# Kernel optimization log

Measured on AMD Instinct MI355X. Metric: run time of the kernel, lower is better.

## Reference

```python
import jax, jax.numpy as jnp
import numpy as np

Q_LEN = 2048
K_LEN = 2048
BATCH = 2
EMBED = 1024
HEADS = 16
HEAD_DIM = EMBED // HEADS
PE_ROWS = 2 * K_LEN


def _shift(p):
    # Transformer-XL pad/flatten shift: p is [B, H, Q, S] with S = 2*K-1 -> [B, H, Q, K]
    B, H, Q, S = p.shape
    pp = jnp.pad(p, ((0, 0), (0, 0), (0, 1), (0, 1)))          # [B,H,Q+1,S+1]
    flat = pp.reshape(B, H, (Q + 1) * (S + 1))
    flat = jax.lax.slice_in_dim(flat, S // 2, S // 2 + Q * S, axis=-1)
    return flat.reshape(B, H, Q, S)[..., : (S + 1) // 2]


def setup_inputs() -> dict:
    key = jax.random.key(0)
    ks = jax.random.split(key, 11)
    ws = 0.02  # weight scale
    inp = {
        "query": jax.random.normal(ks[0], (Q_LEN, BATCH, EMBED), jnp.float32),
        "key": jax.random.normal(ks[1], (K_LEN, BATCH, EMBED), jnp.float32),
        "value": jax.random.normal(ks[2], (K_LEN, BATCH, EMBED), jnp.float32),
        "pe": jax.random.normal(ks[3], (PE_ROWS, EMBED), jnp.float32),
        "w_q": jax.random.normal(ks[4], (EMBED, EMBED), jnp.float32) * ws,
        "w_k": jax.random.normal(ks[5], (EMBED, EMBED), jnp.float32) * ws,
        "w_v": jax.random.normal(ks[6], (EMBED, EMBED), jnp.float32) * ws,
        "w_k_pos": jax.random.normal(ks[7], (EMBED, EMBED), jnp.float32) * ws,
        "out_proj": jax.random.normal(ks[8], (EMBED, EMBED), jnp.float32) * ws,
        "content_bias": jax.random.normal(ks[9], (HEADS, HEAD_DIM), jnp.float32) * ws,
        "pos_bias": jax.random.normal(ks[10], (HEADS, HEAD_DIM), jnp.float32) * ws,
        "attn_mask": jnp.triu(jnp.ones((Q_LEN, K_LEN), dtype=bool), k=1),  # causal
    }
    return inp


def reference(query, key, value, pe, w_q, w_k, w_v, w_k_pos, out_proj,
              content_bias, pos_bias, attn_mask):
    Qlen, B, E = query.shape
    Klen = key.shape[0]
    H, D = content_bias.shape
    scaling = D ** -0.5

    # projections (torch Linear: x @ W^T); layout -> [B, H, L, D]
    q = (query @ w_q.T).reshape(Qlen, B, H, D).transpose(1, 2, 0, 3)
    k = (key @ w_k.T).reshape(Klen, B, H, D).transpose(1, 2, 0, 3)
    v = (value @ w_v.T).reshape(Klen, B, H, D).transpose(1, 2, 0, 3)

    # relative position keys: pe slice of size 2K-1 starting at pe.size(0)//2 - K + 1
    lower = pe.shape[0] // 2 - Klen + 1
    pe_slice = jax.lax.dynamic_slice_in_dim(pe, lower, 2 * Klen - 1, axis=0)
    k_pos = (pe_slice @ w_k_pos.T).reshape(2 * Klen - 1, H, D).transpose(1, 0, 2)  # [H, 2K-1, D]

    content = jnp.einsum('bhqd,bhkd->bhqk', q + content_bias[None, :, None, :], k)
    pos = jnp.einsum('bhqd,hsd->bhqs', q + pos_bias[None, :, None, :], k_pos)
    pos = _shift(pos)  # [B, H, Q, K]

    attn = (content + pos) * scaling
    attn = jnp.where(attn_mask[None, None], -jnp.inf, attn)
    w = jax.nn.softmax(attn, axis=-1)

    out = jnp.einsum('bhqk,bhkd->bhqd', w, v)
    out = out.transpose(2, 0, 1, 3).reshape(Qlen, B, E)
    return out @ out_proj.T
```

## Files before the change

### kernel.cpp

```cpp
#include <hip/hip_runtime.h>
#include <hip/hip_bf16.h>

typedef __hip_bfloat16 bf16;
typedef __attribute__((ext_vector_type(8))) short short8;
typedef __attribute__((ext_vector_type(8))) unsigned short u16x8;
typedef __attribute__((ext_vector_type(4))) float f32x4;

#define QL   2048
#define KLEN 2048
#define BATCH 2
#define EMB  1024
#define NH   16
#define HD   64
#define SPE  4095

__device__ __forceinline__ int detect_f32_wave(const void* __restrict__ p) {
    const ushort4 v = ((const ushort4*)p)[threadIdx.x & 63];
    int c = 0;
    c += __popcll(__ballot(((v.x >> 7) & 0xFF) >= 0x8A));
    c += __popcll(__ballot(((v.y >> 7) & 0xFF) >= 0x8A));
    c += __popcll(__ballot(((v.z >> 7) & 0xFF) >= 0x8A));
    c += __popcll(__ballot(((v.w >> 7) & 0xFF) >= 0x8A));
    return c >= 8;
}

__device__ __forceinline__ ushort4 cvt4(const void* src, long u4i, int f32) {
    ushort4 o;
    if (f32) {
        float4 v = ((const float4*)src)[u4i];
        bf16 a = (bf16)v.x, b = (bf16)v.y, c = (bf16)v.z, e = (bf16)v.w;
        o.x = *(unsigned short*)&a; o.y = *(unsigned short*)&b;
        o.z = *(unsigned short*)&c; o.w = *(unsigned short*)&e;
    } else {
        o = ((const ushort4*)src)[u4i];
    }
    return o;
}

__global__ __launch_bounds__(256) void conv_w(
    const void* w0, const void* w1, const void* w2, const void* w3, const void* w4,
    const void* cb, const void* pb, bf16* __restrict__ wdst)
{
    const int t = threadIdx.x;
    const int bid = blockIdx.x;
    __shared__ int f32s;
    if (bid < 1280) {
        const int seg = bid >> 8, inner = bid & 255;
        const void* src = seg == 0 ? w0 : seg == 1 ? w1 : seg == 2 ? w2 : seg == 3 ? w3 : w4;
        bf16* d = wdst + (size_t)seg * 1048576;
        if (t < 64) { int r = detect_f32_wave(src); if (t == 0) f32s = r; }
        __syncthreads();
        const int f32 = f32s;
#pragma unroll
        for (int i = 0; i < 4; i++) {
            long u4i = (long)inner * 1024 + i * 256 + t;
            ((ushort4*)d)[u4i] = cvt4(src, u4i, f32);
        }
    } else {
        if (t < 64) { int r = detect_f32_wave(cb); if (t == 0) f32s = r; }
        __syncthreads();
        const int f32 = f32s;
        ((ushort4*)(wdst + 5242880))[t]        = cvt4(cb, t, f32);
        ((ushort4*)(wdst + 5242880 + 1024))[t] = cvt4(pb, t, f32);
    }
}

__device__ __forceinline__ void llds16(const bf16* g, bf16* l) {
    __builtin_amdgcn_global_load_lds(
        (const __attribute__((address_space(1))) void*)g,
        (__attribute__((address_space(3))) void*)l,
        16, 0, 0);
}

__device__ __forceinline__ short8 pack_f32x8(const float4& a, const float4& b) {
    short8 o; bf16 x;
    x = (bf16)a.x; o[0] = *(short*)&x;  x = (bf16)a.y; o[1] = *(short*)&x;
    x = (bf16)a.z; o[2] = *(short*)&x;  x = (bf16)a.w; o[3] = *(short*)&x;
    x = (bf16)b.x; o[4] = *(short*)&x;  x = (bf16)b.y; o[5] = *(short*)&x;
    x = (bf16)b.z; o[6] = *(short*)&x;  x = (bf16)b.w; o[7] = *(short*)&x;
    return o;
}

template<bool F32>
struct AStage {
    u16x8  u[2];
    float4 f[2][2];
    __device__ __forceinline__ void load(const void* Av, const int go[2], int k0) {
#pragma unroll
        for (int i = 0; i < 2; i++) {
            int e = go[i] + k0;
            if (F32) {
                const float4* F = (const float4*)Av;
                f[i][0] = F[e >> 2];
                f[i][1] = F[(e >> 2) + 1];
            } else {
                u[i] = ((const u16x8*)Av)[e >> 3];
            }
        }
    }
    __device__ __forceinline__ void write(bf16* dst, int t) {
#pragma unroll
        for (int i = 0; i < 2; i++) {
            int c = i * 256 + t;
            short8 v;
            if (F32) v = pack_f32x8(f[i][0], f[i][1]);
            else     v = *(short8*)&u[i];
            *(short8*)&dst[c * 8] = v;
        }
    }
};

__device__ __forceinline__ void gcompute(
    const bf16* As, const bf16* Ws, int wr, int wc, int lm, int quad,
    f32x4 acc[4][8])
{
    short8 af[4], wf[8];
#pragma unroll
    for (int x = 0; x < 4; x++) {
        int ra = wr + x * 16 + lm;
        af[x] = *(const short8*)&As[ra * 32 + ((quad ^ (ra & 3)) * 8)];
    }
#pragma unroll
    for (int y = 0; y < 8; y++) {
        int rb = wc + y * 16 + lm;
        wf[y] = *(const short8*)&Ws[rb * 32 + ((quad ^ (rb & 3)) * 8)];
    }
#pragma unroll
    for (int mt = 0; mt < 4; mt++)
#pragma unroll
        for (int nt = 0; nt < 8; nt++)
            acc[mt][nt] = __builtin_amdgcn_mfma_f32_16x16x32_bf16(
                af[mt], wf[nt], acc[mt][nt], 0, 0, 0);
}

#define GWB() do { asm volatile("s_waitcnt vmcnt(0) lgkmcnt(0)" ::: "memory"); \
    __builtin_amdgcn_s_barrier(); __builtin_amdgcn_sched_barrier(0); } while (0)
#define GLB() do { asm volatile("s_waitcnt lgkmcnt(0)" ::: "memory"); \
    __builtin_amdgcn_s_barrier(); __builtin_amdgcn_sched_barrier(0); } while (0)

template<bool F32>
__device__ void gloop(
    const void* Av, const bf16* W, int m0, int n0, int mode,
    bf16* Asd0, bf16* Asd1, bf16* Wsd0, bf16* Wsd1,
    int t, int wr, int wc, int lm, int quad, f32x4 acc[4][8])
{
    int go[2];
#pragma unroll
    for (int i = 0; i < 2; i++) {
        int c = i * 256 + t, r = c >> 2, gc = (c & 3) ^ (r & 3);
        int ar = m0 + r;
        if (mode == 3) { ar = ar + 1; if (ar > 4095) ar = 4095; }
        go[i] = ar * 1024 + gc * 8;
    }
    auto stageW = [&](bf16* dst, int k0) {
#pragma unroll
        for (int i = 0; i < 4; i++) {
            int c = i * 256 + t, r = c >> 2, gc = (c & 3) ^ (r & 3);
            llds16(W + (size_t)(n0 + r) * 1024 + k0 + gc * 8, dst + (c & ~63) * 8);
        }
    };

    AStage<F32> sa, sb;
    sa.load(Av, go, 0);
    stageW(Wsd0, 0);

#pragma unroll 1
    for (int tt = 0; tt < 32; tt += 2) {
        GWB();
        sa.write(Asd0, t);
        GLB();
        sb.load(Av, go, (tt + 1) * 32);
        stageW(Wsd1, (tt + 1) * 32);
        gcompute(Asd0, Wsd0, wr, wc, lm, quad, acc);

        GWB();
        sb.write(Asd1, t);
        GLB();
        if (tt + 2 < 32) {
            sa.load(Av, go, (tt + 2) * 32);
            stageW(Wsd0, (tt + 2) * 32);
        }
        gcompute(Asd1, Wsd1, wr, wc, lm, quad, acc);
    }
}

__global__ __launch_bounds__(256, 2) void gemm_big(
    const void* __restrict__ Aq, const void* __restrict__ Ak,
    const void* __restrict__ Avv, const void* __restrict__ Ape,
    const bf16* __restrict__ ao, const bf16* __restrict__ wslab,
    bf16* __restrict__ qc, bf16* __restrict__ qp,
    bf16* __restrict__ kw, bf16* __restrict__ vw,
    bf16* __restrict__ kpos, float* __restrict__ outf, int mode_base)
{
    const int o = blockIdx.x;
    const int mode = mode_base + (o >> 7);
    const int s = (o >> 3) & 15;
    const int bx = (o & 7) + 8 * (s & 3);
    const int by = s >> 2;

    const void* A = mode == 0 ? Aq : mode == 1 ? Ak : mode == 2 ? Avv :
                    mode == 3 ? Ape : (const void*)ao;
    const bf16* W = wslab + (size_t)mode * 1048576;

    __shared__ __align__(16) bf16 Asd[2][128 * 32];
    __shared__ __align__(16) bf16 Wsd[2][256 * 32];
    __shared__ int f32s;

    const int t = threadIdx.x;
    const int w = t >> 6, lane = t & 63, lm = lane & 15, quad = lane >> 4;
    const int m0 = bx * 128, n0 = by * 256;
    const int wr = (w >> 1) * 64, wc = (w & 1) * 128;

    if (t < 64) { int r = detect_f32_wave(A); if (t == 0) f32s = r; }
    __syncthreads();

    f32x4 acc[4][8] = {};

    if (f32s) gloop<true >(A, W, m0, n0, mode, Asd[0], Asd[1], Wsd[0], Wsd[1],
                           t, wr, wc, lm, quad, acc);
    else      gloop<false>(A, W, m0, n0, mode, Asd[0], Asd[1], Wsd[0], Wsd[1],
                           t, wr, wc, lm, quad, acc);

    const bf16* cbb = wslab + 5242880;
    const bf16* pbb = wslab + 5242880 + 1024;

#pragma unroll
    for (int mt = 0; mt < 4; mt++) {
#pragma unroll
        for (int nt = 0; nt < 8; nt++) {
#pragma unroll
            for (int r4 = 0; r4 < 4; r4++) {
                int row = m0 + wr + mt * 16 + quad * 4 + r4;
                int col = n0 + wc + nt * 16 + lm;
                float v = acc[mt][nt][r4];
                if (mode == 0) {
                    int l = row >> 1, b = row & 1;
                    int h = col >> 6, d = col & 63;
                    size_t idx = ((size_t)(b * NH + h) * QL + l) * HD + d;
                    qc[idx] = (bf16)(v + __bfloat162float(cbb[col]));
                    qp[idx] = (bf16)(v + __bfloat162float(pbb[col]));
                } else if (mode == 1) {
                    int l = row >> 1, b = row & 1;
                    int h = col >> 6, d = col & 63;
                    kw[((size_t)(b * NH + h) * KLEN + l) * HD + d] = (bf16)v;
                } else if (mode == 2) {
                    int l = row >> 1, b = row & 1;
                    int h = col >> 6, d = col & 63;
                    vw[((size_t)(b * NH + h) * KLEN + l) * HD + d] = (bf16)v;
                } else if (mode == 3) {
                    if (row < SPE) {
                        int h = col >> 6, d = col & 63;
                        kpos[((size_t)h * SPE + row) * HD + d] = (bf16)v;
                    }
                } else {
                    outf[(size_t)row * 1024 + col] = v;
                }
            }
        }
    }
}

#define NEG_INF (-1.0e30f)
#define SCL2 0.18033688011f

__global__ __launch_bounds__(256) void attn_mfma(
    const bf16* __restrict__ qc_g, const bf16* __restrict__ qp_g,
    const bf16* __restrict__ k_g,  const bf16* __restrict__ v_g,
    const bf16* __restrict__ kpos_g, bf16* __restrict__ ao)
{
    const int lin = blockIdx.x + (blockIdx.y << 6) + (blockIdx.z << 10);
    const int xcd = lin & 7, s = lin >> 3;
    const int g   = (xcd << 2) | (s >> 6);
    const int u   = s & 63;
    const int bx  = 63 - u;
    const int h   = g & 15;
    const int b   = g >> 4;
    const int q0  = bx * 32;

    const bf16* qc_bh  = qc_g + ((size_t)(b * NH + h) * QL) * HD;
    const bf16* qp_bh  = qp_g + ((size_t)(b * NH + h) * QL) * HD;
    const bf16* k_bh   = k_g  + ((size_t)(b * NH + h) * KLEN) * HD;
    const bf16* v_bh   = v_g  + ((size_t)(b * NH + h) * KLEN) * HD;
    const bf16* kpos_h = kpos_g + (size_t)h * SPE * HD;

    __shared__ __align__(16) bf16 K_s [64 * 64];
    __shared__ __align__(16) bf16 Kp_s[96 * 64];
    __shared__ __align__(16) bf16 Vt_s[64 * 64];
    __shared__ __align__(16) bf16 Pb_s[32 * 64];
    __shared__ float Sc_s[32][69];
    __shared__ float Pt_s[32][98];
    __shared__ float arow_s[32];

    const int t = threadIdx.x;
    const int w = t >> 6, lane = t & 63, lm = lane & 15, quad = lane >> 4;

    const int sr = t >> 3;
    const int sc = (t & 7) * 8;
    const int vrr = t >> 3, vch = t & 7;
    const int vkc = vrr >> 2;

    const int mtc = w & 1;
    const int ntc = (w >> 1) * 2;
    const int mtp = w >> 1;
    const int ntp = (w & 1) * 3;

    float m_run = NEG_INF, l_part = 0.0f;
    f32x4 accO[2] = {{0,0,0,0},{0,0,0,0}};
    u16x8 vv0, vv1;

    const int nkt = (bx >> 1) + 1;

    short8 aQc0, aQc1, aQp0, aQp1;
    {
        const bf16* qr = qc_bh + (size_t)(q0 + mtc * 16 + lm) * HD;
        aQc0 = *(const short8*)(qr + quad * 8);
        aQc1 = *(const short8*)(qr + (4 + quad) * 8);
        const bf16* pr = qp_bh + (size_t)(q0 + mtp * 16 + lm) * HD;
        aQp0 = *(const short8*)(pr + quad * 8);
        aQp1 = *(const short8*)(pr + (4 + quad) * 8);
    }

#pragma unroll
    for (int i = 0; i < 2; i++) {
        int c = i * 256 + t, r = c >> 3, ch = c & 7, gc = ch ^ (r & 7);
        llds16(k_bh + (size_t)r * HD + gc * 8, K_s + (c & ~63) * 8);
    }
    {
        const int s0 = 2016 - q0;
#pragma unroll
        for (int i = 0; i < 3; i++) {
            int c = i * 256 + t, r = c >> 3, ch = c & 7, gc = ch ^ (r & 7);
            llds16(kpos_h + (size_t)(s0 + r) * HD + gc * 8, Kp_s + (c & ~63) * 8);
        }
    }
    vv0 = *(const u16x8*)&v_bh[(size_t)(2 * vrr)     * HD + vch * 8];
    vv1 = *(const u16x8*)&v_bh[(size_t)(2 * vrr + 1) * HD + vch * 8];

    for (int kt = 0; kt < nkt; kt++) {
        const int k0 = kt * 64;

        __syncthreads();

        {
            const int off = (2 * vrr) & 7;
#pragma unroll
            for (int j = 0; j < 8; j++) {
                unsigned int pair = (unsigned int)vv0[j] | ((unsigned int)vv1[j] << 16);
                int slot = vkc ^ vch ^ j;
                *(unsigned int*)&Vt_s[(vch * 8 + j) * 64 + slot * 8 + off] = pair;
            }
        }

        {
#pragma unroll
            for (int n = 0; n < 2; n++) {
                int rowB = (ntc + n) * 16 + lm;
                short8 b0 = *(const short8*)&K_s[rowB * 64 + ((quad)     ^ (rowB & 7)) * 8];
                short8 b1 = *(const short8*)&K_s[rowB * 64 + ((4 + quad) ^ (rowB & 7)) * 8];
                f32x4 acc = {0, 0, 0, 0};
                acc = __builtin_amdgcn_mfma_f32_16x16x32_bf16(aQc0, b0, acc, 0, 0, 0);
                acc = __builtin_amdgcn_mfma_f32_16x16x32_bf16(aQc1, b1, acc, 0, 0, 0);
#pragma unroll
                for (int r = 0; r < 4; r++)
                    Sc_s[mtc * 16 + quad * 4 + r][(ntc + n) * 16 + lm] = acc[r];
            }
        }
        {
#pragma unroll
            for (int n = 0; n < 3; n++) {
                int rowB = (ntp + n) * 16 + lm;
                short8 b0 = *(const short8*)&Kp_s[rowB * 64 + ((quad)     ^ (rowB & 7)) * 8];
                short8 b1 = *(const short8*)&Kp_s[rowB * 64 + ((4 + quad) ^ (rowB & 7)) * 8];
                f32x4 acc = {0, 0, 0, 0};
                acc = __builtin_amdgcn_mfma_f32_16x16x32_bf16(aQp0, b0, acc, 0, 0, 0);
                acc = __builtin_amdgcn_mfma_f32_16x16x32_bf16(aQp1, b1, acc, 0, 0, 0);
#pragma unroll
                for (int r = 0; r < 4; r++)
                    Pt_s[mtp * 16 + quad * 4 + r][(ntp + n) * 16 + lm] = acc[r];
            }
        }

        __syncthreads();

        if (kt + 1 < nkt) {
            const int k0n = k0 + 64;
            const int s0n = k0n - q0 + 2016;
#pragma unroll
            for (int i = 0; i < 2; i++) {
                int c = i * 256 + t, r = c >> 3, ch = c & 7, gc = ch ^ (r & 7);
                llds16(k_bh + (size_t)(k0n + r) * HD + gc * 8, K_s + (c & ~63) * 8);
            }
#pragma unroll
            for (int i = 0; i < 3; i++) {
                int c = i * 256 + t, r = c >> 3, ch = c & 7, gc = ch ^ (r & 7);
                llds16(kpos_h + (size_t)(s0n + r) * HD + gc * 8, Kp_s + (c & ~63) * 8);
            }
            vv0 = *(const u16x8*)&v_bh[(size_t)(k0n + 2 * vrr)     * HD + vch * 8];
            vv1 = *(const u16x8*)&v_bh[(size_t)(k0n + 2 * vrr + 1) * HD + vch * 8];
        }

        {
            float p[8];
            float pmax = NEG_INF;
#pragma unroll
            for (int j = 0; j < 8; j++) {
                int col = sc + j;
                float sv = (Sc_s[sr][col] + Pt_s[sr][col - sr + 31]) * SCL2;
                if (k0 + col > q0 + sr) sv = NEG_INF;
                p[j] = sv;
                pmax = fmaxf(pmax, sv);
            }
            float alpha = 1.0f;
            if (!__all(pmax <= m_run + 11.5f)) {
                float mx = pmax;
                mx = fmaxf(mx, __shfl_xor(mx, 1, 8));
                mx = fmaxf(mx, __shfl_xor(mx, 2, 8));
                mx = fmaxf(mx, __shfl_xor(mx, 4, 8));
                float mnew = fmaxf(m_run, mx);
                alpha = __builtin_amdgcn_exp2f(m_run - mnew);
                m_run = mnew;
            }
            float ls = 0.0f;
#pragma unroll
            for (int j = 0; j < 8; j++) {
                p[j] = __builtin_amdgcn_exp2f(p[j] - m_run);
                ls += p[j];
            }
            l_part = l_part * alpha + ls;
            if ((t & 7) == 0) arow_s[sr] = alpha;
            short8 pv;
#pragma unroll
            for (int j = 0; j < 8; j++) { bf16 x = (bf16)p[j]; pv[j] = *(short*)&x; }
            *(short8*)&Pb_s[sr * 64 + ((t & 7) ^ (sr & 7)) * 8] = pv;
        }

        asm volatile("s_waitcnt lgkmcnt(0)" ::: "memory");
        __builtin_amdgcn_s_barrier();
        __builtin_amdgcn_sched_barrier(0);

        {
            float al[4];
#pragma unroll
            for (int r = 0; r < 4; r++) al[r] = arow_s[mtc * 16 + quad * 4 + r];
            int rowA = mtc * 16 + lm;
            short8 a0 = *(const short8*)&Pb_s[rowA * 64 + ((quad)     ^ (rowA & 7)) * 8];
            short8 a1 = *(const short8*)&Pb_s[rowA * 64 + ((4 + quad) ^ (rowA & 7)) * 8];
#pragma unroll
            for (int n = 0; n < 2; n++) {
                int d = (ntc + n) * 16 + lm;
                int ds = (d >> 3) ^ (d & 7);
                short8 b0 = *(const short8*)&Vt_s[d * 64 + ((quad     ^ ds)) * 8];
                short8 b1 = *(const short8*)&Vt_s[d * 64 + (((4 + quad) ^ ds)) * 8];
#pragma unroll
                for (int r = 0; r < 4; r++) accO[n][r] *= al[r];
                accO[n] = __builtin_amdgcn_mfma_f32_16x16x32_bf16(a0, b0, accO[n], 0, 0, 0);
                accO[n] = __builtin_amdgcn_mfma_f32_16x16x32_bf16(a1, b1, accO[n], 0, 0, 0);
            }
        }
    }

    l_part += __shfl_xor(l_part, 1, 8);
    l_part += __shfl_xor(l_part, 2, 8);
    l_part += __shfl_xor(l_part, 4, 8);

    __syncthreads();
    if ((t & 7) == 0) arow_s[sr] = l_part;
    __syncthreads();

    float linv[4];
#pragma unroll
    for (int r = 0; r < 4; r++) linv[r] = 1.0f / arow_s[mtc * 16 + quad * 4 + r];
#pragma unroll
    for (int n = 0; n < 2; n++) {
#pragma unroll
        for (int r = 0; r < 4; r++) {
            int row = mtc * 16 + quad * 4 + r;
            ao[(((size_t)(q0 + row) * BATCH + b) * EMB) + h * HD + (ntc + n) * 16 + lm] =
                (bf16)(accO[n][r] * linv[r]);
        }
    }
}

extern "C" void kernel_launch(void* const* d_in, const int* in_sizes, int n_in,
                              void* d_out, int out_size, void* d_ws, size_t ws_size,
                              hipStream_t stream)
{
    const void* query = d_in[0];
    const void* key   = d_in[1];
    const void* value = d_in[2];
    const void* pe    = d_in[3];
    const void* w_q   = d_in[4];
    const void* w_k   = d_in[5];
    const void* w_v   = d_in[6];
    const void* w_kp  = d_in[7];
    const void* w_out = d_in[8];
    const void* cb    = d_in[9];
    const void* pb    = d_in[10];
    float* out = (float*)d_out;

    const size_t SLAB = 4194304;
    bf16* qc   = (bf16*)d_ws;
    bf16* qp   = qc + SLAB;
    bf16* kw   = qp + SLAB;
    bf16* vw   = kw + SLAB;
    bf16* kpos = vw + SLAB;
    bf16* ao   = kpos + SLAB;
    bf16* wqb  = ao + SLAB;

    dim3 blk(256);

    conv_w<<<dim3(1281), blk, 0, stream>>>(w_q, w_k, w_v, w_kp, w_out, cb, pb, wqb);

    gemm_big<<<dim3(512), blk, 0, stream>>>(
        query, key, value, pe, nullptr, wqb, qc, qp, kw, vw, kpos, nullptr, 0);

    attn_mfma<<<dim3(64, NH, BATCH), blk, 0, stream>>>(qc, qp, kw, vw, kpos, ao);

    gemm_big<<<dim3(128), blk, 0, stream>>>(
        query, key, value, pe, ao, wqb, qc, qp, kw, vw, kpos, out, 4);
}
```

Before: 355.6 us.

## Triple-buffer GEMM LDS stages with prefetch distance two and one barrier per step

Replaces the double-buffered projection GEMM main loop with a three-slot LDS ring that prefetches two K-steps ahead. It uses partial vmcnt waits so only the oldest loads must land, and needs one barrier per iteration instead of two. The aim is to hide global-load latency and cut synchronisation stalls. In exchange it uses more LDS (24 KB to 36 KB), which may limit the two-blocks-per-CU occupancy target, and it depends on the hard-coded vmcnt counts matching the number of outstanding loads.

```diff
diff --git a/kernel.cpp b/kernel.cpp
--- a/kernel.cpp
+++ b/kernel.cpp
@@ -133,15 +133,10 @@
                 af[mt], wf[nt], acc[mt][nt], 0, 0, 0);
 }
 
-#define GWB() do { asm volatile("s_waitcnt vmcnt(0) lgkmcnt(0)" ::: "memory"); \
-    __builtin_amdgcn_s_barrier(); __builtin_amdgcn_sched_barrier(0); } while (0)
-#define GLB() do { asm volatile("s_waitcnt lgkmcnt(0)" ::: "memory"); \
-    __builtin_amdgcn_s_barrier(); __builtin_amdgcn_sched_barrier(0); } while (0)
-
 template<bool F32>
 __device__ void gloop(
     const void* Av, const bf16* W, int m0, int n0, int mode,
-    bf16* Asd0, bf16* Asd1, bf16* Wsd0, bf16* Wsd1,
+    bf16* AsdB, bf16* WsdB,
     int t, int wr, int wc, int lm, int quad, f32x4 acc[4][8])
 {
     int go[2];
@@ -160,27 +155,33 @@
         }
     };
 
-    AStage<F32> sa, sb;
-    sa.load(Av, go, 0);
-    stageW(Wsd0, 0);
+    AStage<F32> s0, s1;
+    s0.load(Av, go, 0);   stageW(WsdB,            0);
+    s1.load(Av, go, 32);  stageW(WsdB + 256 * 32, 32);
 
 #pragma unroll 1
-    for (int tt = 0; tt < 32; tt += 2) {
-        GWB();
-        sa.write(Asd0, t);
-        GLB();
-        sb.load(Av, go, (tt + 1) * 32);
-        stageW(Wsd1, (tt + 1) * 32);
-        gcompute(Asd0, Wsd0, wr, wc, lm, quad, acc);
-
-        GWB();
-        sb.write(Asd1, t);
-        GLB();
-        if (tt + 2 < 32) {
-            sa.load(Av, go, (tt + 2) * 32);
-            stageW(Wsd0, (tt + 2) * 32);
-        }
-        gcompute(Asd1, Wsd1, wr, wc, lm, quad, acc);
+    for (int it = 0; it < 32; ++it) {
+        const int cur = it % 3;
+        bf16* Ac = AsdB + cur * (128 * 32);
+        bf16* Wc = WsdB + cur * (256 * 32);
+
+        if (it == 31)       asm volatile("s_waitcnt vmcnt(0)" ::: "memory");
+        else if constexpr (F32) asm volatile("s_waitcnt vmcnt(8)" ::: "memory");
+        else                asm volatile("s_waitcnt vmcnt(6)" ::: "memory");
+
+        if (it & 1) s1.write(Ac, t); else s0.write(Ac, t);
+
+        asm volatile("s_waitcnt lgkmcnt(0)" ::: "memory");
+        __builtin_amdgcn_s_barrier();
+        __builtin_amdgcn_sched_barrier(0);
+
+        if (it + 2 < 32) {
+            const int nb = (it + 2) % 3;
+            if (it & 1) s1.load(Av, go, (it + 2) * 32);
+            else        s0.load(Av, go, (it + 2) * 32);
+            stageW(WsdB + nb * (256 * 32), (it + 2) * 32);
+        }
+        gcompute(Ac, Wc, wr, wc, lm, quad, acc);
     }
 }
 
@@ -202,8 +203,8 @@
                     mode == 3 ? Ape : (const void*)ao;
     const bf16* W = wslab + (size_t)mode * 1048576;
 
-    __shared__ __align__(16) bf16 Asd[2][128 * 32];
-    __shared__ __align__(16) bf16 Wsd[2][256 * 32];
+    __shared__ __align__(16) bf16 Asd[3][128 * 32];
+    __shared__ __align__(16) bf16 Wsd[3][256 * 32];
     __shared__ int f32s;
 
     const int t = threadIdx.x;
@@ -216,9 +217,9 @@
 
     f32x4 acc[4][8] = {};
 
-    if (f32s) gloop<true >(A, W, m0, n0, mode, Asd[0], Asd[1], Wsd[0], Wsd[1],
+    if (f32s) gloop<true >(A, W, m0, n0, mode, &Asd[0][0], &Wsd[0][0],
                            t, wr, wc, lm, quad, acc);
-    else      gloop<false>(A, W, m0, n0, mode, Asd[0], Asd[1], Wsd[0], Wsd[1],
+    else      gloop<false>(A, W, m0, n0, mode, &Asd[0][0], &Wsd[0][0],
                            t, wr, wc, lm, quad, acc);
 
     const bf16* cbb = wslab + 5242880;
```

New measurement: 384.2 us. 8.0% more time.
